# Kernel optimization log

Hardware: AMD Instinct MI355X
Metric: run time of the kernel (lower is better)

The kernel has to match this reference:

```python
import jax, jax.numpy as jnp
import numpy as np


def setup_inputs() -> dict:
    key = jax.random.key(0)
    ks = jax.random.split(key, 5)
    B, TOTAL_IN, GROUPS, IN_NUM, OUT = 500000, 200, 25, 8, 75
    x = jax.random.normal(ks[0], (B, TOTAL_IN), dtype=jnp.float32)
    w1 = jax.random.normal(ks[1], (IN_NUM, 1), dtype=jnp.float32) * 0.35
    b1 = jax.random.normal(ks[2], (1,), dtype=jnp.float32) * 0.1
    w2 = jax.random.normal(ks[3], (1, 3), dtype=jnp.float32) * 0.5
    b2 = jax.random.normal(ks[4], (3,), dtype=jnp.float32) * 0.1
    # in_out_map: 25 groups, each gathers 8 input cols and scatters 3 output cols
    in_out_k = jnp.arange(GROUPS * IN_NUM, dtype=jnp.int32).reshape(GROUPS, IN_NUM)
    in_out_v = jnp.arange(GROUPS * 3, dtype=jnp.int32).reshape(GROUPS, 3)
    return {"x": x, "w1": w1, "b1": b1, "w2": w2, "b2": b2,
            "in_out_k": in_out_k, "in_out_v": in_out_v}


def reference(x, w1, b1, w2, b2, in_out_k, in_out_v):
    B = x.shape[0]
    OUT = 75
    # Batched gather of all groups at once: [B, G, IN_NUM]
    g = x[:, in_out_k]
    # Shared tiny MLP applied to every group: Linear(IN_NUM,1) -> ReLU -> Linear(1,3)
    h = jax.nn.relu(jnp.einsum('bgi,io->bgo', g, w1) + b1)   # [B, G, 1]
    o = jnp.einsum('bgo,ot->bgt', h, w2) + b2                 # [B, G, 3]
    # Scatter group outputs into the [B, 75] output (zeros elsewhere)
    out = jnp.zeros((B, OUT), dtype=x.dtype)
    out = out.at[:, in_out_v.reshape(-1)].set(o.reshape(B, -1))
    return out
```

## Files before the change

### kernel.cpp

```cpp
#include <hip/hip_runtime.h>


#define GROUPS  25
#define IN_NUM  8
#define ROW     200
#define OUTROW  75
#define OUTT    3

__global__ __launch_bounds__(256) void mlp_rsna6_kernel(
    const float* __restrict__ x,
    const float* __restrict__ w1,
    const float* __restrict__ b1,
    const float* __restrict__ w2,
    const float* __restrict__ b2,
    const int*   __restrict__ iok,
    const int*   __restrict__ iov,
    float*       __restrict__ out,
    int total)
{
    int t = blockIdx.x * blockDim.x + threadIdx.x;
    if (t >= total) return;

    int b = t / GROUPS;
    int g = t - b * GROUPS;

    int kbase = iok[g * IN_NUM];
    int vbase = iov[g * OUTT];

    const float4* xp = reinterpret_cast<const float4*>(
        x + (size_t)b * ROW + kbase);
    float4 a0 = xp[0];
    float4 a1 = xp[1];

    float s = b1[0];
    s = fmaf(a0.x, w1[0], s);
    s = fmaf(a0.y, w1[1], s);
    s = fmaf(a0.z, w1[2], s);
    s = fmaf(a0.w, w1[3], s);
    s = fmaf(a1.x, w1[4], s);
    s = fmaf(a1.y, w1[5], s);
    s = fmaf(a1.z, w1[6], s);
    s = fmaf(a1.w, w1[7], s);
    float h = fmaxf(s, 0.0f);

    float* op = out + (size_t)b * OUTROW + vbase;
    op[0] = fmaf(h, w2[0], b2[0]);
    op[1] = fmaf(h, w2[1], b2[1]);
    op[2] = fmaf(h, w2[2], b2[2]);
}

extern "C" void kernel_launch(void* const* d_in, const int* in_sizes, int n_in,
                              void* d_out, int out_size, void* d_ws, size_t ws_size,
                              hipStream_t stream) {
    const float* x   = (const float*)d_in[0];
    const float* w1  = (const float*)d_in[1];
    const float* b1  = (const float*)d_in[2];
    const float* w2  = (const float*)d_in[3];
    const float* b2  = (const float*)d_in[4];
    const int*   iok = (const int*)d_in[5];
    const int*   iov = (const int*)d_in[6];
    float*       out = (float*)d_out;

    int B = in_sizes[0] / ROW;
    int total = B * GROUPS;

    int block = 256;
    int grid = (total + block - 1) / block;
    mlp_rsna6_kernel<<<grid, block, 0, stream>>>(
        x, w1, b1, w2, b2, iok, iov, out, total);
}
```

Baseline: 559.8 us.

## Stage row tiles in shared memory for coalesced loads and stores

Each block now loads 32 full input rows into LDS with contiguous float4 reads, computes all group outputs into an LDS output tile, then writes the tile back with coalesced float4 stores. This replaces per-thread strided gathers and scattered 3-float stores, which wasted memory bandwidth. Weights are hoisted into registers. It costs about 35KB of LDS per block, which may limit occupancy, and adds two barriers with no overlap between loading and compute.

```diff
diff --git a/kernel.cpp b/kernel.cpp
--- a/kernel.cpp
+++ b/kernel.cpp
@@ -6,8 +6,10 @@
 #define ROW     200
 #define OUTROW  75
 #define OUTT    3
+#define RPB     32
+#define THREADS 256
 
-__global__ __launch_bounds__(256) void mlp_rsna6_kernel(
+__global__ __launch_bounds__(THREADS) void mlp_rsna6_kernel(
     const float* __restrict__ x,
     const float* __restrict__ w1,
     const float* __restrict__ b1,
@@ -16,37 +18,72 @@
     const int*   __restrict__ iok,
     const int*   __restrict__ iov,
     float*       __restrict__ out,
-    int total)
+    int nrows)
 {
-    int t = blockIdx.x * blockDim.x + threadIdx.x;
-    if (t >= total) return;
+    __shared__ float xs[RPB * ROW];
+    __shared__ float os[RPB * OUTROW];
+    __shared__ int   kb_s[GROUPS];
+    __shared__ int   vb_s[GROUPS];
 
-    int b = t / GROUPS;
-    int g = t - b * GROUPS;
+    const int tid = threadIdx.x;
+    const int r0  = blockIdx.x * RPB;
+    const int rows = min(RPB, nrows - r0);
 
-    int kbase = iok[g * IN_NUM];
-    int vbase = iov[g * OUTT];
+    if (tid < GROUPS) {
+        kb_s[tid] = iok[tid * IN_NUM];
+        vb_s[tid] = iov[tid * OUTT];
+    }
 
-    const float4* xp = reinterpret_cast<const float4*>(
-        x + (size_t)b * ROW + kbase);
-    float4 a0 = xp[0];
-    float4 a1 = xp[1];
+    const float4* xg  = reinterpret_cast<const float4*>(x + (size_t)r0 * ROW);
+    float4*       xs4 = reinterpret_cast<float4*>(xs);
+    const int n4 = rows * (ROW / 4);
+    for (int i = tid; i < n4; i += THREADS) xs4[i] = xg[i];
 
-    float s = b1[0];
-    s = fmaf(a0.x, w1[0], s);
-    s = fmaf(a0.y, w1[1], s);
-    s = fmaf(a0.z, w1[2], s);
-    s = fmaf(a0.w, w1[3], s);
-    s = fmaf(a1.x, w1[4], s);
-    s = fmaf(a1.y, w1[5], s);
-    s = fmaf(a1.z, w1[6], s);
-    s = fmaf(a1.w, w1[7], s);
-    float h = fmaxf(s, 0.0f);
+    const float W10 = w1[0], W11 = w1[1], W12 = w1[2], W13 = w1[3];
+    const float W14 = w1[4], W15 = w1[5], W16 = w1[6], W17 = w1[7];
+    const float B1  = b1[0];
+    const float W20 = w2[0], W21 = w2[1], W22 = w2[2];
+    const float B20 = b2[0], B21 = b2[1], B22 = b2[2];
 
-    float* op = out + (size_t)b * OUTROW + vbase;
-    op[0] = fmaf(h, w2[0], b2[0]);
-    op[1] = fmaf(h, w2[1], b2[1]);
-    op[2] = fmaf(h, w2[2], b2[2]);
+    __syncthreads();
+
+    const int items = rows * GROUPS;
+    for (int i = tid; i < items; i += THREADS) {
+        int bl = i / GROUPS;
+        int g  = i - bl * GROUPS;
+        int kb = kb_s[g];
+        int vb = vb_s[g];
+
+        const float4* xp = reinterpret_cast<const float4*>(&xs[bl * ROW + kb]);
+        float4 a0 = xp[0];
+        float4 a1 = xp[1];
+
+        float s = B1;
+        s = fmaf(a0.x, W10, s);
+        s = fmaf(a0.y, W11, s);
+        s = fmaf(a0.z, W12, s);
+        s = fmaf(a0.w, W13, s);
+        s = fmaf(a1.x, W14, s);
+        s = fmaf(a1.y, W15, s);
+        s = fmaf(a1.z, W16, s);
+        s = fmaf(a1.w, W17, s);
+        float h = fmaxf(s, 0.0f);
+
+        float* op = &os[bl * OUTROW + vb];
+        op[0] = fmaf(h, W20, B20);
+        op[1] = fmaf(h, W21, B21);
+        op[2] = fmaf(h, W22, B22);
+    }
+
+    __syncthreads();
+
+    float4*       og  = reinterpret_cast<float4*>(out + (size_t)r0 * OUTROW);
+    const float4* os4 = reinterpret_cast<const float4*>(os);
+    const int fl  = rows * OUTROW;
+    const int m4  = fl / 4;
+    for (int i = tid; i < m4; i += THREADS) og[i] = os4[i];
+    for (int i = m4 * 4 + tid; i < fl; i += THREADS)
+        out[(size_t)r0 * OUTROW + i] = os[i];
 }
 
 extern "C" void kernel_launch(void* const* d_in, const int* in_sizes, int n_in,
@@ -61,11 +98,8 @@
     const int*   iov = (const int*)d_in[6];
     float*       out = (float*)d_out;
 
-    int B = in_sizes[0] / ROW;
-    int total = B * GROUPS;
-
-    int block = 256;
-    int grid = (total + block - 1) / block;
-    mlp_rsna6_kernel<<<grid, block, 0, stream>>>(
-        x, w1, b1, w2, b2, iok, iov, out, total);
+    int nrows = in_sizes[0] / ROW;
+    int grid  = (nrows + RPB - 1) / RPB;
+    mlp_rsna6_kernel<<<grid, THREADS, 0, stream>>>(
+        x, w1, b1, w2, b2, iok, iov, out, nrows);
 }
```

Measured after the change: 568.6 us. No clear change (+1.6%).
